# Kernel optimization log

Hardware: AMD Instinct MI355X
Metric: run time of the kernel (lower is better)

The kernel has to match this reference:

```python
import jax, jax.numpy as jnp
import numpy as np

# FP4 E2M1 constants (from the torch module)
EXP_BITS = 2
EXP_BIAS = 1          # 2**(EXP_BITS-1) - 1
MANT_BITS = 1
MAX_EXP_FIELD = 3     # (1 << EXP_BITS) - 1
MIN_NORMAL_EXP = 0    # 1 - EXP_BIAS
FP4_MAX = 6.0         # (1 + 1/2) * 2**(MAX_EXP_FIELD-1 - EXP_BIAS + 1) = 1.5 * 4
GROUP = 128


def fp4_quant_dequant(x):
    """Faithful composition of _float_to_fp4 followed by _fp4_to_float (E2M1,
    subnormal-aware), expressed in float arithmetic (bit pack/unpack cancels)."""
    a = jnp.abs(x)
    zero_mask = a == 0
    a_safe = jnp.where(zero_mask, jnp.float32(1e-8), a)
    e = jnp.floor(jnp.log2(a_safe))                      # unbiased exponent
    is_sub = e < MIN_NORMAL_EXP
    e_c = jnp.clip(e, MIN_NORMAL_EXP, MAX_EXP_FIELD - EXP_BIAS)
    mant_scale = float(1 << MANT_BITS)                   # 2.0
    mant_normal = jnp.clip(jnp.round((a_safe / jnp.exp2(e_c) - 1.0) * mant_scale), 0.0, mant_scale - 1.0)
    mant_sub = jnp.clip(jnp.round(a_safe / (2.0 ** MIN_NORMAL_EXP) * mant_scale), 0.0, mant_scale - 1.0)
    mant = jnp.where(is_sub, mant_sub, mant_normal)
    # decode (_fp4_to_float): normals (1 + m/2)*2^(e), subnormals (m/2)*2^(1-bias)
    val_normal = (1.0 + mant / mant_scale) * jnp.exp2(e_c)
    val_sub = (mant / mant_scale) * (2.0 ** (1 - EXP_BIAS))
    val = jnp.where(is_sub, val_sub, val_normal)
    val = jnp.where(x < 0, -val, val)
    return jnp.where(zero_mask, jnp.zeros_like(val), val)


def setup_inputs() -> dict:
    key = jax.random.key(0)
    k1, k2, k3 = jax.random.split(key, 3)
    x = jax.random.normal(k1, (4096, 4096), dtype=jnp.float32)
    weight = jax.random.normal(k2, (4096, 4096), dtype=jnp.float32) * 0.02
    b = jax.random.normal(k3, (4096,), dtype=jnp.float32)
    return {"x": x, "weight": weight, "b": b}


def reference(x, weight, b):
    out_f, in_f = weight.shape
    wg = weight.reshape(out_f, in_f // GROUP, GROUP)
    amax = jnp.max(jnp.abs(wg), axis=-1, keepdims=True)       # [out, groups, 1]
    scale = jnp.where(amax == 0, jnp.float32(1.0), amax / FP4_MAX)
    w_deq = (fp4_quant_dequant(wg / scale) * scale).reshape(out_f, in_f)
    return x @ w_deq.T + b
```

## Files before the change

kernel.cpp:

```cpp
#include <hip/hip_runtime.h>
#include <hip/hip_bf16.h>
#include <stdint.h>

#define KDIM 4096
#define NDIM 4096
#define MDIM 4096
#define BM 256
#define BN 256
#define BK 64

typedef __attribute__((ext_vector_type(8))) short bf16x8;
typedef __attribute__((ext_vector_type(4))) float f32x4;


__device__ __forceinline__ unsigned short bf16bits(float f) {
    union { float f; uint32_t u; } c; c.f = f;
    uint32_t u = c.u;
    uint32_t r = (u + 0x7fffu + ((u >> 16) & 1u)) >> 16;
    return (unsigned short)r;
}

__device__ __forceinline__ float fp4qd(float x) {
    float a = fabsf(x);
    if (a == 0.0f) return 0.0f;
    float e = floorf(log2f(a));
    float val;
    if (e < 0.0f) {
        float mant = fminf(fmaxf(rintf(a * 2.0f), 0.0f), 1.0f);
        val = mant * 0.5f;
    } else {
        float ec = fminf(e, 2.0f);
        float p  = exp2f(ec);
        float mant = fminf(fmaxf(rintf((a / p - 1.0f) * 2.0f), 0.0f), 1.0f);
        val = (1.0f + 0.5f * mant) * p;
    }
    return (x < 0.0f) ? -val : val;
}

__device__ __forceinline__ void gld16(void* lds, const void* g) {
    __builtin_amdgcn_global_load_lds(
        (const __attribute__((address_space(1))) unsigned int*)g,
        (__attribute__((address_space(3))) unsigned int*)lds,
        16, 0, 0);
}

__global__ __launch_bounds__(256) void prep_kernel(const float* __restrict__ X,
                                                   const float* __restrict__ W,
                                                   unsigned short* __restrict__ Xb,
                                                   char* __restrict__ Wq2) {
    int bid = blockIdx.x;
    int tid = threadIdx.x;
    if (bid < 16384) {
        size_t i = ((size_t)bid * 256 + tid) * 4;
        float4 v = *(const float4*)(X + i);
        ushort4 o;
        o.x = bf16bits(v.x); o.y = bf16bits(v.y);
        o.z = bf16bits(v.z); o.w = bf16bits(v.w);
        *(ushort4*)(Xb + i) = o;
    } else {
        int bw = bid - 16384;
        int rb = bw >> 3;
        int kb = bw & 7;
        int row = rb * 16 + (tid >> 4);
        int kq  = tid & 15;
        int k0  = kb * 512 + kq * 32;
        const float* src = W + (size_t)row * KDIM + k0;

        float v[32];
        float am = 0.f;
        #pragma unroll
        for (int j = 0; j < 8; ++j) {
            float4 f = *(const float4*)(src + j * 4);
            v[j*4+0] = f.x; v[j*4+1] = f.y; v[j*4+2] = f.z; v[j*4+3] = f.w;
            am = fmaxf(am, fmaxf(fmaxf(fabsf(f.x), fabsf(f.y)),
                                 fmaxf(fabsf(f.z), fabsf(f.w))));
        }
        am = fmaxf(am, __shfl_xor(am, 1));
        am = fmaxf(am, __shfl_xor(am, 2));
        float scale = (am == 0.0f) ? 1.0f : am / 6.0f;

        const int c   = row >> 6;
        const int nf  = (row >> 4) & 3;
        const int r15 = row & 15;
        #pragma unroll
        for (int g = 0; g < 4; ++g) {
            uint32_t u[4];
            #pragma unroll
            for (int p = 0; p < 4; ++p) {
                float q0 = fp4qd(v[g*8 + p*2    ] / scale) * scale;
                float q1 = fp4qd(v[g*8 + p*2 + 1] / scale) * scale;
                u[p] = (uint32_t)bf16bits(q0) | ((uint32_t)bf16bits(q1) << 16);
            }
            int k8    = (k0 >> 3) + g;
            int kt    = k8 >> 3;
            int kk8   = k8 & 7;
            int ks    = kk8 >> 2;
            int kslot = kk8 & 3;
            size_t addr = ((size_t)((kt * 64 + c) * 8 + nf + ks * 4) << 10)
                        + (size_t)((kslot * 16 + r15) << 4);
            uint4 o = make_uint4(u[0], u[1], u[2], u[3]);
            *(uint4*)(Wq2 + addr) = o;
        }
    }
}


#define BAR()    __builtin_amdgcn_s_barrier()
#define LGKM0()  asm volatile("s_waitcnt lgkmcnt(0)" ::: "memory")
#define VM0()    asm volatile("s_waitcnt vmcnt(0)" ::: "memory")
#define SCH0()   __builtin_amdgcn_sched_barrier(0)
#define PRIO(x)  __builtin_amdgcn_s_setprio(x)

__global__ __launch_bounds__(512, 2) void gemm256(const unsigned short* __restrict__ A,
                                                  const char* __restrict__ Bq,
                                                  const float* __restrict__ bias,
                                                  float* __restrict__ C) {
    __shared__ __attribute__((aligned(16))) char smem[2][32768];
    char* sm = (char*)&smem[0][0];

    const int t = threadIdx.x;
    const int l = t & 63;
    const int w = __builtin_amdgcn_readfirstlane(t >> 6);
    const int wm = w >> 2;
    const int wn = w & 3;

    int bid = blockIdx.x;
    int swz = (bid & 7) * 32 + (bid >> 3);
    int brow = (swz >> 4) * BM;
    int bcol = (swz & 15) * BN;

    const int lr8  = l >> 3;
    const int slot = l & 7;
    const int scol = (slot ^ lr8) << 3;
    const unsigned short* pA = A + (size_t)(brow + w * 8 + lr8) * KDIM + scol;

#define STAGE_A(b, h, kt) do {                                                 \
    const unsigned short* _s = pA + (size_t)(h) * 128 * KDIM + (size_t)(kt) * BK; \
    gld16(sm + (b) * 32768 + (h) * 16384 + w * 1024, _s);                      \
    gld16(sm + (b) * 32768 + (h) * 16384 + 8192 + w * 1024,                    \
          _s + (size_t)64 * KDIM);                                             \
} while (0)
#define STAGE4(b, kt) do { STAGE_A(b, 0, kt); STAGE_A(b, 1, kt); } while (0)

    const int fr  = l & 15;
    const int fq  = l >> 4;
    const int kx0 = ((fq    ) ^ (fr & 7)) << 4;
    const int kx1 = ((fq + 4) ^ (fr & 7)) << 4;
    const int frA = fr * 128;

#define RD_A(b, mh) do {                                                        \
    const char* _p = sm + (b) * 32768 + wm * 16384 + (mh) * 8192 + frA;         \
    _Pragma("unroll")                                                           \
    for (int m = 0; m < 4; ++m) {                                               \
        av[m][0] = *(const bf16x8*)(_p + m * 2048 + kx0);                       \
        av[m][1] = *(const bf16x8*)(_p + m * 2048 + kx1);                       \
    }                                                                           \
} while (0)

    const char* pBq = Bq + ((size_t)(bcol >> 6) + wn) * 8192 + (size_t)l * 16;

#define GLB_B(arr, kt) do {                                                     \
    const char* _b = pBq + (size_t)(kt) * 524288;                               \
    arr[0][0] = *(const bf16x8*)(_b          );                                 \
    arr[1][0] = *(const bf16x8*)(_b + 1024   );                                 \
    arr[2][0] = *(const bf16x8*)(_b + 2048   );                                 \
    arr[3][0] = *(const bf16x8*)(_b + 3072   );                                 \
    arr[0][1] = *(const bf16x8*)(_b + 4096   );                                 \
    arr[1][1] = *(const bf16x8*)(_b + 5120   );                                 \
    arr[2][1] = *(const bf16x8*)(_b + 6144   );                                 \
    arr[3][1] = *(const bf16x8*)(_b + 7168   );                                 \
} while (0)

#define MMH(mh, B_)                                                             \
    _Pragma("unroll")                                                           \
    for (int m = 0; m < 4; ++m)                                                 \
        _Pragma("unroll")                                                       \
        for (int nf = 0; nf < 4; ++nf)                                          \
            _Pragma("unroll")                                                   \
            for (int ks = 0; ks < 2; ++ks)                                      \
                acc[(mh) * 4 + m][nf] =                                         \
                    __builtin_amdgcn_mfma_f32_16x16x32_bf16(                    \
                        av[m][ks], B_[nf][ks], acc[(mh) * 4 + m][nf], 0, 0, 0);

    f32x4 acc[8][4];
    #pragma unroll
    for (int m = 0; m < 8; ++m)
        #pragma unroll
        for (int n = 0; n < 4; ++n)
            acc[m][n] = f32x4{0.f, 0.f, 0.f, 0.f};

    bf16x8 av[4][2], bEv[4][2], bOd[4][2];

    GLB_B(bEv, 0);
    STAGE4(0, 0);

    for (int it = 0; it < 32; ++it) {
        const int kO  = 2 * it + 1;
        const int kE2 = (2 * it + 2) & 63;

        VM0(); BAR(); SCH0();
        RD_A(0, 0);
        GLB_B(bOd, kO);
        STAGE4(1, kO);
        LGKM0(); SCH0();
        PRIO(1); MMH(0, bEv); PRIO(0); SCH0();
        RD_A(0, 1);
        LGKM0(); SCH0();
        PRIO(1); MMH(1, bEv); PRIO(0);

        VM0(); BAR(); SCH0();
        RD_A(1, 0);
        GLB_B(bEv, kE2);
        STAGE4(0, kE2);
        LGKM0(); SCH0();
        PRIO(1); MMH(0, bOd); PRIO(0); SCH0();
        RD_A(1, 1);
        LGKM0(); SCH0();
        PRIO(1); MMH(1, bOd); PRIO(0);
    }

    float bb[4];
    #pragma unroll
    for (int n = 0; n < 4; ++n) bb[n] = bias[bcol + wn * 64 + n * 16 + fr];
    #pragma unroll
    for (int mi = 0; mi < 8; ++mi) {
        #pragma unroll
        for (int q = 0; q < 4; ++q) {
            int row = brow + wm * 128 + mi * 16 + fq * 4 + q;
            float* crow = C + (size_t)row * NDIM + bcol + wn * 64;
            #pragma unroll
            for (int n = 0; n < 4; ++n)
                crow[n * 16 + fr] = acc[mi][n][q] + bb[n];
        }
    }
}

extern "C" void kernel_launch(void* const* d_in, const int* in_sizes, int n_in,
                              void* d_out, int out_size, void* d_ws, size_t ws_size,
                              hipStream_t stream) {
    const float* x = (const float*)d_in[0];
    const float* w = (const float*)d_in[1];
    const float* b = (const float*)d_in[2];
    float* out = (float*)d_out;

    unsigned short* xb = (unsigned short*)d_ws;
    char* wq2 = (char*)d_ws + (size_t)NDIM * KDIM * 2;

    prep_kernel<<<16384 + 2048, 256, 0, stream>>>(x, w, xb, wq2);
    gemm256<<<(MDIM / BM) * (NDIM / BN), 512, 0, stream>>>(xb, wq2, b, out);
}
```

Baseline: 168.2 us.

## Deepen GEMM pipeline to four LDS buffers with partial vmcnt waits

Grows the shared-memory A staging from two to four 32KB buffers so each A tile is prefetched two K-steps ahead. The full vmcnt(0) drains are replaced by vmcnt(20), letting later global loads stay in flight. The MFMA loop order is also changed to iterate ks outermost. The cost is 128KB of LDS per block, which likely cuts resident blocks per CU below the launch-bounds target of two, and a hand-counted vmcnt that must match the number of outstanding loads.

```diff
diff --git a/kernel.cpp b/kernel.cpp
--- a/kernel.cpp
+++ b/kernel.cpp
@@ -107,6 +107,7 @@
 
 #define BAR()    __builtin_amdgcn_s_barrier()
 #define LGKM0()  asm volatile("s_waitcnt lgkmcnt(0)" ::: "memory")
+#define VM20()   asm volatile("s_waitcnt vmcnt(20)" ::: "memory")
 #define VM0()    asm volatile("s_waitcnt vmcnt(0)" ::: "memory")
 #define SCH0()   __builtin_amdgcn_sched_barrier(0)
 #define PRIO(x)  __builtin_amdgcn_s_setprio(x)
@@ -115,7 +116,7 @@
                                                   const char* __restrict__ Bq,
                                                   const float* __restrict__ bias,
                                                   float* __restrict__ C) {
-    __shared__ __attribute__((aligned(16))) char smem[2][32768];
+    __shared__ __attribute__((aligned(16))) char smem[4][32768];
     char* sm = (char*)&smem[0][0];
 
     const int t = threadIdx.x;
@@ -134,13 +135,12 @@
     const int scol = (slot ^ lr8) << 3;
     const unsigned short* pA = A + (size_t)(brow + w * 8 + lr8) * KDIM + scol;
 
-#define STAGE_A(b, h, kt) do {                                                 \
+#define S_A(b, h, kt) do {                                                     \
     const unsigned short* _s = pA + (size_t)(h) * 128 * KDIM + (size_t)(kt) * BK; \
     gld16(sm + (b) * 32768 + (h) * 16384 + w * 1024, _s);                      \
     gld16(sm + (b) * 32768 + (h) * 16384 + 8192 + w * 1024,                    \
           _s + (size_t)64 * KDIM);                                             \
 } while (0)
-#define STAGE4(b, kt) do { STAGE_A(b, 0, kt); STAGE_A(b, 1, kt); } while (0)
 
     const int fr  = l & 15;
     const int fq  = l >> 4;
@@ -161,23 +161,23 @@
 
 #define GLB_B(arr, kt) do {                                                     \
     const char* _b = pBq + (size_t)(kt) * 524288;                               \
-    arr[0][0] = *(const bf16x8*)(_b          );                                 \
-    arr[1][0] = *(const bf16x8*)(_b + 1024   );                                 \
-    arr[2][0] = *(const bf16x8*)(_b + 2048   );                                 \
-    arr[3][0] = *(const bf16x8*)(_b + 3072   );                                 \
-    arr[0][1] = *(const bf16x8*)(_b + 4096   );                                 \
-    arr[1][1] = *(const bf16x8*)(_b + 5120   );                                 \
-    arr[2][1] = *(const bf16x8*)(_b + 6144   );                                 \
-    arr[3][1] = *(const bf16x8*)(_b + 7168   );                                 \
+    arr[0][0] = *(const bf16x8*)(_b       );                                    \
+    arr[1][0] = *(const bf16x8*)(_b + 1024);                                    \
+    arr[2][0] = *(const bf16x8*)(_b + 2048);                                    \
+    arr[3][0] = *(const bf16x8*)(_b + 3072);                                    \
+    arr[0][1] = *(const bf16x8*)(_b + 4096);                                    \
+    arr[1][1] = *(const bf16x8*)(_b + 5120);                                    \
+    arr[2][1] = *(const bf16x8*)(_b + 6144);                                    \
+    arr[3][1] = *(const bf16x8*)(_b + 7168);                                    \
 } while (0)
 
 #define MMH(mh, B_)                                                             \
     _Pragma("unroll")                                                           \
-    for (int m = 0; m < 4; ++m)                                                 \
+    for (int ks = 0; ks < 2; ++ks)                                              \
         _Pragma("unroll")                                                       \
-        for (int nf = 0; nf < 4; ++nf)                                          \
+        for (int m = 0; m < 4; ++m)                                             \
             _Pragma("unroll")                                                   \
-            for (int ks = 0; ks < 2; ++ks)                                      \
+            for (int nf = 0; nf < 4; ++nf)                                      \
                 acc[(mh) * 4 + m][nf] =                                         \
                     __builtin_amdgcn_mfma_f32_16x16x32_bf16(                    \
                         av[m][ks], B_[nf][ks], acc[(mh) * 4 + m][nf], 0, 0, 0);
@@ -189,34 +189,35 @@
         for (int n = 0; n < 4; ++n)
             acc[m][n] = f32x4{0.f, 0.f, 0.f, 0.f};
 
-    bf16x8 av[4][2], bEv[4][2], bOd[4][2];
-
-    GLB_B(bEv, 0);
-    STAGE4(0, 0);
-
-    for (int it = 0; it < 32; ++it) {
-        const int kO  = 2 * it + 1;
-        const int kE2 = (2 * it + 2) & 63;
-
-        VM0(); BAR(); SCH0();
-        RD_A(0, 0);
-        GLB_B(bOd, kO);
-        STAGE4(1, kO);
-        LGKM0(); SCH0();
-        PRIO(1); MMH(0, bEv); PRIO(0); SCH0();
-        RD_A(0, 1);
-        LGKM0(); SCH0();
-        PRIO(1); MMH(1, bEv); PRIO(0);
-
-        VM0(); BAR(); SCH0();
-        RD_A(1, 0);
-        GLB_B(bEv, kE2);
-        STAGE4(0, kE2);
-        LGKM0(); SCH0();
-        PRIO(1); MMH(0, bOd); PRIO(0); SCH0();
-        RD_A(1, 1);
-        LGKM0(); SCH0();
-        PRIO(1); MMH(1, bOd); PRIO(0);
+    bf16x8 av[4][2], bE[4][2], bO[4][2];
+
+    S_A(0, 0, 0); S_A(0, 1, 0); S_A(1, 0, 1); S_A(1, 1, 1);
+    GLB_B(bE, 0); GLB_B(bO, 1);
+    VM0();
+    BAR(); SCH0();
+
+#define TILE_K(j, BREG, kidx) do {                                              \
+                                  \
+    RD_A(j, 0); S_A((j + 2) & 3, 0, kidx);                                      \
+    BAR(); LGKM0(); SCH0();                                                     \
+    PRIO(1); MMH(0, BREG); PRIO(0);                                            \
+             \
+    RD_A(j, 1); S_A((j + 2) & 3, 1, kidx);                                      \
+    BAR(); LGKM0(); SCH0();                                                     \
+    PRIO(1); MMH(1, BREG); PRIO(0);                                            \
+    GLB_B(BREG, kidx);                                                          \
+    VM20();                                                                     \
+} while (0)
+
+    for (int it = 0; it < 16; ++it) {
+        const int kt2 = (4 * it + 2) & 63;
+        const int kt3 = (4 * it + 3) & 63;
+        const int kt4 = (4 * it + 4) & 63;
+        const int kt5 = (4 * it + 5) & 63;
+        TILE_K(0, bE, kt2);
+        TILE_K(1, bO, kt3);
+        TILE_K(2, bE, kt4);
+        TILE_K(3, bO, kt5);
     }
 
     float bb[4];
```

Result: faster. 163.4 us (-2.9%).
